# Optimization experiments

Measured on AMD Instinct MI355X. Metric: run time of the kernel, lower is better.

The kernel has to match this reference:

```python
import jax, jax.numpy as jnp
import numpy as np

H, E, DFF = 768, 8, 3072
B, S = 2, 1024


def setup_inputs() -> dict:
    key = jax.random.key(0)
    ks = jax.random.split(key, 4)
    scale = 1.0 / np.sqrt(H)
    return {
        "x": jax.random.normal(ks[0], (B, S, H), dtype=jnp.float32),
        "Wg": jax.random.normal(ks[1], (H, E), dtype=jnp.float32) * scale,
        "bg": jnp.zeros((E,), dtype=jnp.float32),
        "W1": jax.random.normal(ks[2], (E, H, DFF), dtype=jnp.float32) * scale,
        "b1": jnp.zeros((E, DFF), dtype=jnp.float32),
        "W2": jax.random.normal(ks[3], (E, DFF, H), dtype=jnp.float32) * (1.0 / np.sqrt(DFF)),
        "b2": jnp.zeros((E, H), dtype=jnp.float32),
        "top_k": 2,
    }


def reference(x, Wg, bg, W1, b1, W2, b2, top_k):
    b, s, h = x.shape
    xf = x.reshape(-1, h)                       # [T, H]
    logits = xf @ Wg + bg                        # [T, E]
    probs = jax.nn.softmax(logits, axis=-1)
    w, idx = jax.lax.top_k(probs, top_k)         # [T, K]
    w = w / jnp.sum(w, axis=-1, keepdims=True)   # renormalize top-k weights
    # dense combine weights per (token, expert): [T, E]
    comb = jnp.sum(jax.nn.one_hot(idx, W1.shape[0], dtype=xf.dtype) * w[..., None], axis=1)
    # per-expert MLP: Linear -> exact GELU -> Linear
    hmid = jax.nn.gelu(jnp.einsum('th,ehf->etf', xf, W1) + b1[:, None, :], approximate=False)
    eo = jnp.einsum('etf,efh->eth', hmid, W2) + b2[:, None, :]   # [E, T, H]
    out = jnp.einsum('te,eth->th', comb, eo)     # weighted combine
    return out.reshape(b, s, h)
```

## Files before the change

### kernel.cpp

```cpp
#include <hip/hip_runtime.h>
#include <hip/hip_bf16.h>
#include <math.h>

#define H_DIM 768
#define E_NUM 8
#define DFF   3072
#define T_NUM 2048
#define PAIRS 4096

typedef __attribute__((ext_vector_type(8))) short          s16x8;
typedef __attribute__((ext_vector_type(4))) float          f32x4;
typedef __attribute__((ext_vector_type(4))) unsigned int   u32x4;
typedef __attribute__((ext_vector_type(4))) unsigned short u16x4;
typedef __attribute__((ext_vector_type(8))) unsigned short u16x8;

__device__ __forceinline__ unsigned short f2bf(float f) {
  unsigned int u = __builtin_bit_cast(unsigned int, f);
  u += 0x7FFFu + ((u >> 16) & 1u);
  return (unsigned short)(u >> 16);
}

__device__ __forceinline__ float bf2f(unsigned short v) {
  unsigned int u = ((unsigned int)v) << 16;
  return __builtin_bit_cast(float, u);
}

__device__ __forceinline__ float gelu_fast(float x) {
  float t = x * x;
  float a = __builtin_fmaf(t, -0.10294221f, -2.3022082f);
  float w;
  asm("v_exp_f32 %0, %1" : "=v"(w) : "v"(x * a));
  float r;
  float d = 1.0f + w;
  asm("v_rcp_f32 %0, %1" : "=v"(r) : "v"(d));
  return x * r;
}


__device__ __forceinline__ void route_body(
    int rb, const float* __restrict__ x, const float* __restrict__ Wg,
    const float* __restrict__ bg, int* __restrict__ eidx, float* __restrict__ ew) {
  int wave = threadIdx.x >> 6, lane = threadIdx.x & 63;
  int t = rb * 4 + wave;
  const float* xr = x + (size_t)t * H_DIM;
  float acc[E_NUM];
#pragma unroll
  for (int e = 0; e < E_NUM; ++e) acc[e] = 0.f;
#pragma unroll
  for (int i = 0; i < H_DIM / 64; ++i) {
    int h = i * 64 + lane;
    float xv = xr[h];
    f32x4 w0 = *(const f32x4*)&Wg[h * 8];
    f32x4 w1 = *(const f32x4*)&Wg[h * 8 + 4];
    acc[0] += xv * w0[0]; acc[1] += xv * w0[1];
    acc[2] += xv * w0[2]; acc[3] += xv * w0[3];
    acc[4] += xv * w1[0]; acc[5] += xv * w1[1];
    acc[6] += xv * w1[2]; acc[7] += xv * w1[3];
  }
#pragma unroll
  for (int e = 0; e < E_NUM; ++e) {
#pragma unroll
    for (int off = 32; off > 0; off >>= 1) acc[e] += __shfl_xor(acc[e], off);
  }
  if (lane == 0) {
    float l[E_NUM];
#pragma unroll
    for (int e = 0; e < E_NUM; ++e) l[e] = acc[e] + bg[e];
    int i0 = 0;
#pragma unroll
    for (int e = 1; e < E_NUM; ++e) if (l[e] > l[i0]) i0 = e;
    int i1 = (i0 == 0) ? 1 : 0;
#pragma unroll
    for (int e = 0; e < E_NUM; ++e) if (e != i0 && l[e] > l[i1]) i1 = e;
    float d  = expf(l[i1] - l[i0]);
    eidx[2 * t]     = i0;
    eidx[2 * t + 1] = i1;
    ew[2 * t]       = 1.f / (1.f + d);
    ew[2 * t + 1]   = d / (1.f + d);
  }
}

__device__ __forceinline__ void transpose_body(
    int tb, const float* __restrict__ in, unsigned short* __restrict__ out,
    int R, int C) {
  __shared__ unsigned short tile[64][72];
  int e   = tb / ((R / 64) * (C / 64));
  int rem = tb % ((R / 64) * (C / 64));
  int bx  = rem % (C / 64);
  int by  = rem / (C / 64);
  int c0 = bx * 64, r0 = by * 64;
  const float* ip = in + (size_t)e * R * C;
  unsigned short* op = out + (size_t)e * R * C;
  int tid = threadIdx.x;
  int tx = tid & 15, ty = tid >> 4;
#pragma unroll
  for (int i = 0; i < 4; ++i) {
    int r = ty + 16 * i;
    f32x4 v = *(const f32x4*)&ip[(size_t)(r0 + r) * C + c0 + tx * 4];
    u16x4 o;
    o[0] = f2bf(v[0]); o[1] = f2bf(v[1]); o[2] = f2bf(v[2]); o[3] = f2bf(v[3]);
    *(u16x4*)&tile[r][tx * 4] = o;
  }
  __syncthreads();
  int c  = tid & 63;
  int rc = (tid >> 6) * 16;
#pragma unroll
  for (int h = 0; h < 2; ++h) {
    u16x8 o;
#pragma unroll
    for (int j = 0; j < 8; ++j) o[j] = tile[rc + h * 8 + j][c];
    *(u16x8*)&op[(size_t)(c0 + c) * R + r0 + rc + h * 8] = o;
  }
}

__device__ __forceinline__ void gather_body(
    int gb, const float* __restrict__ x, const int* __restrict__ tok_of,
    unsigned short* __restrict__ Xg) {
  int s = gb * 4 + (threadIdx.x >> 6);
  int lane = threadIdx.x & 63;
  int t = tok_of[s];
  const f32x4* xr = (const f32x4*)(x + (size_t)t * H_DIM);
  u16x4* orow = (u16x4*)(Xg + (size_t)s * H_DIM);
#pragma unroll
  for (int i = 0; i < H_DIM / 256; ++i) {
    f32x4 v = xr[i * 64 + lane];
    u16x4 o;
    o[0] = f2bf(v[0]); o[1] = f2bf(v[1]); o[2] = f2bf(v[2]); o[3] = f2bf(v[3]);
    orow[i * 64 + lane] = o;
  }
}


__global__ __launch_bounds__(256) void k_route_t1(
    const float* __restrict__ x, const float* __restrict__ Wg,
    const float* __restrict__ bg, int* __restrict__ eidx, float* __restrict__ ew,
    const float* __restrict__ W1, unsigned short* __restrict__ Wb1) {
  int b = blockIdx.x;
  if (b < T_NUM / 4) route_body(b, x, Wg, bg, eidx, ew);
  else               transpose_body(b - T_NUM / 4, W1, Wb1, H_DIM, DFF);
}

__global__ __launch_bounds__(256) void k_gather_t2(
    const float* __restrict__ x, const int* __restrict__ tok_of,
    unsigned short* __restrict__ Xg,
    const float* __restrict__ W2, unsigned short* __restrict__ Wb2) {
  int b = blockIdx.x;
  if (b < PAIRS / 4) gather_body(b, x, tok_of, Xg);
  else               transpose_body(b - PAIRS / 4, W2, Wb2, DFF, H_DIM);
}

__global__ __launch_bounds__(256) void k_build(
    const int* __restrict__ eidx, int* __restrict__ counts, int* __restrict__ offsets,
    int* __restrict__ tok_of, int* __restrict__ slot_of) {
  __shared__ int cnt[E_NUM];
  __shared__ int cur[E_NUM];
  int tid = threadIdx.x;
  if (tid < E_NUM) cnt[tid] = 0;
  __syncthreads();
#pragma unroll
  for (int i = 0; i < PAIRS / 256; ++i)
    atomicAdd(&cnt[eidx[i * 256 + tid]], 1);
  __syncthreads();
  if (tid == 0) {
    int s = 0;
    for (int e = 0; e < E_NUM; ++e) { cur[e] = s; s += cnt[e]; }
  }
  __syncthreads();
  if (tid < E_NUM) { counts[tid] = cnt[tid]; offsets[tid] = cur[tid]; }
#pragma unroll
  for (int i = 0; i < PAIRS / 256; ++i) {
    int p = i * 256 + tid;
    int s = atomicAdd(&cur[eidx[p]], 1);
    tok_of[s] = p >> 1;
    slot_of[p] = s;
  }
}

template <int KTOT, int NT, int NSPLIT, int MT_MAX, bool GELU_OUT>
__global__ __launch_bounds__(256) void k_gemm(
    const unsigned short* __restrict__ A, const unsigned short* __restrict__ B,
    const float* __restrict__ bias, void* __restrict__ C,
    const int* __restrict__ counts, const int* __restrict__ offsets) {
  constexpr int NDIM  = NT * 128;
  constexpr int KLEN  = KTOT / NSPLIT;
  constexpr int NSTEP = KLEN / 64;
  int l = blockIdx.x;
  int nt = l % NT;  l /= NT;
  int e  = l & 7;   l >>= 3;
  int part = l % NSPLIT;
  int mt = l / NSPLIT;
  int Me = counts[e];
  if (mt * 128 >= Me) return;
  int seg = offsets[e];

  __shared__ __align__(16) unsigned short Al[2][128 * 64];
  __shared__ __align__(16) unsigned short Bl[2][128 * 64];

  int tid  = threadIdx.x;
  int lane = tid & 63;
  int wave = tid >> 6;
  int wm = wave >> 1, wn = wave & 1;

  int sr   = tid >> 3;
  int scl  = (tid & 7) * 8;
  int scs  = (((tid & 7) ^ (sr & 7)) * 8);
  int rxor = (lane & 7) << 3;

  f32x4 acc[4][4];
#pragma unroll
  for (int m = 0; m < 4; ++m)
#pragma unroll
    for (int n = 0; n < 4; ++n) acc[m][n] = (f32x4){0.f, 0.f, 0.f, 0.f};

  const unsigned short* Abase = A + (size_t)seg * KTOT;
  const unsigned short* Bbase = B + (size_t)e * NDIM * KTOT + (size_t)(nt * 128) * KTOT;
  const int kbeg = part * KLEN;

  auto stage = [&](int bb, int k0) {
#pragma unroll
    for (int j = 0; j < 4; ++j) {
      int row = j * 32 + sr;
      int r = mt * 128 + row;
      r = (r < Me) ? r : (Me - 1);
      const unsigned short* gp = Abase + (size_t)r * KTOT + k0 + scs;
      __builtin_amdgcn_global_load_lds(
          (__attribute__((address_space(1))) void*)gp,
          (__attribute__((address_space(3))) void*)&Al[bb][row * 64 + scl], 16, 0, 0);
    }
#pragma unroll
    for (int j = 0; j < 4; ++j) {
      int row = j * 32 + sr;
      const unsigned short* gp = Bbase + (size_t)row * KTOT + k0 + scs;
      __builtin_amdgcn_global_load_lds(
          (__attribute__((address_space(1))) void*)gp,
          (__attribute__((address_space(3))) void*)&Bl[bb][row * 64 + scl], 16, 0, 0);
    }
  };

  auto compute = [&](int bb) {
#pragma unroll
    for (int kk = 0; kk < 2; ++kk) {
      int ko = kk * 32 + (lane >> 4) * 8;
      s16x8 af[4], bfr[4];
#pragma unroll
      for (int m = 0; m < 4; ++m) {
        int row = wm * 64 + m * 16 + (lane & 15);
        u32x4 v = *(const u32x4*)&Al[bb][(row * 64 + ko) ^ rxor];
        af[m] = __builtin_bit_cast(s16x8, v);
      }
#pragma unroll
      for (int n = 0; n < 4; ++n) {
        int row = wn * 64 + n * 16 + (lane & 15);
        u32x4 v = *(const u32x4*)&Bl[bb][(row * 64 + ko) ^ rxor];
        bfr[n] = __builtin_bit_cast(s16x8, v);
      }
#pragma unroll
      for (int m = 0; m < 4; ++m)
#pragma unroll
        for (int n = 0; n < 4; ++n)
          acc[m][n] = __builtin_amdgcn_mfma_f32_16x16x32_bf16(af[m], bfr[n], acc[m][n], 0, 0, 0);
    }
  };

  stage(0, kbeg);
  stage(1, kbeg + 64);
  int cur = 0;
#pragma unroll
  for (int s = 0; s < NSTEP; ++s) {
    if (s + 1 < NSTEP) asm volatile("s_waitcnt vmcnt(8)" ::: "memory");
    else               asm volatile("s_waitcnt vmcnt(0)" ::: "memory");
    __builtin_amdgcn_s_barrier();
    compute(cur);
    if (s + 2 < NSTEP) {
      __builtin_amdgcn_s_barrier();
      stage(cur, kbeg + (s + 2) * 64);
    }
    cur ^= 1;
  }

  int rbase = mt * 128 + wm * 64;
  int cbase = nt * 128 + wn * 64;
#pragma unroll
  for (int m = 0; m < 4; ++m) {
#pragma unroll
    for (int n = 0; n < 4; ++n) {
      int col = cbase + n * 16 + (lane & 15);
      float bv = GELU_OUT ? bias[e * NDIM + col] : 0.f;
#pragma unroll
      for (int r = 0; r < 4; ++r) {
        int row = rbase + m * 16 + (lane >> 4) * 4 + r;
        if (row < Me) {
          float v = acc[m][n][r] + bv;
          size_t idx = ((size_t)part * PAIRS + seg + row) * NDIM + col;
          if constexpr (GELU_OUT) {
            ((unsigned short*)C)[idx] = f2bf(gelu_fast(v));
          } else {
            ((unsigned short*)C)[idx] = f2bf(v);
          }
        }
      }
    }
  }
}

template <int NSPLIT>
__global__ void k_combine(const unsigned short* __restrict__ P, const int* __restrict__ slot_of,
                          const int* __restrict__ eidx, const float* __restrict__ ew,
                          const float* __restrict__ b2, float* __restrict__ out) {
  int t = blockIdx.x;
  int i = threadIdx.x;
  int s0 = slot_of[2 * t], s1 = slot_of[2 * t + 1];
  int e0 = eidx[2 * t],    e1 = eidx[2 * t + 1];
  float w0 = ew[2 * t], w1 = ew[2 * t + 1];
  f32x4 a = *(const f32x4*)&b2[e0 * H_DIM + i * 4];
  f32x4 c = *(const f32x4*)&b2[e1 * H_DIM + i * 4];
#pragma unroll
  for (int p = 0; p < NSPLIT; ++p) {
    u16x4 va = *(const u16x4*)&P[((size_t)p * PAIRS + s0) * H_DIM + i * 4];
    u16x4 vb = *(const u16x4*)&P[((size_t)p * PAIRS + s1) * H_DIM + i * 4];
#pragma unroll
    for (int j = 0; j < 4; ++j) { a[j] += bf2f(va[j]); c[j] += bf2f(vb[j]); }
  }
  f32x4 o;
  o[0] = w0 * a[0] + w1 * c[0];
  o[1] = w0 * a[1] + w1 * c[1];
  o[2] = w0 * a[2] + w1 * c[2];
  o[3] = w0 * a[3] + w1 * c[3];
  ((f32x4*)(out + (size_t)t * H_DIM))[i] = o;
}

extern "C" void kernel_launch(void* const* d_in, const int* in_sizes, int n_in,
                              void* d_out, int out_size, void* d_ws, size_t ws_size,
                              hipStream_t stream) {
  (void)in_sizes; (void)n_in; (void)out_size;
  const float* x  = (const float*)d_in[0];
  const float* Wg = (const float*)d_in[1];
  const float* bg = (const float*)d_in[2];
  const float* W1 = (const float*)d_in[3];
  const float* b1 = (const float*)d_in[4];
  const float* W2 = (const float*)d_in[5];
  const float* b2 = (const float*)d_in[6];
  float* out = (float*)d_out;

  char* w = (char*)d_ws;
  size_t off = 0;
  auto take = [&](size_t n) { void* p = w + off; off = (off + n + 255) & ~(size_t)255; return p; };
  int*   ctrl    = (int*)  take(64 * sizeof(int));
  int*   eidx    = (int*)  take(PAIRS * sizeof(int));
  float* ew      = (float*)take(PAIRS * sizeof(float));
  int*   slot_of = (int*)  take(PAIRS * sizeof(int));
  int*   tok_of  = (int*)  take(PAIRS * sizeof(int));
  unsigned short* Xg   = (unsigned short*)take((size_t)PAIRS * H_DIM * 2);
  unsigned short* Hmid = (unsigned short*)take((size_t)PAIRS * DFF * 2);
  unsigned short* P    = (unsigned short*)take((size_t)3 * PAIRS * H_DIM * 2);
  unsigned short* Wb1  = (unsigned short*)take((size_t)E_NUM * H_DIM * DFF * 2);
  unsigned short* Wb2  = (unsigned short*)take((size_t)E_NUM * H_DIM * DFF * 2);
  if (off > ws_size) return;

  int* counts  = ctrl;
  int* offsets = ctrl + 8;

  k_route_t1<<<T_NUM / 4 + E_NUM * (H_DIM / 64) * (DFF / 64), 256, 0, stream>>>(
      x, Wg, bg, eidx, ew, W1, Wb1);
  k_build<<<1, 256, 0, stream>>>(eidx, counts, offsets, tok_of, slot_of);
  k_gather_t2<<<PAIRS / 4 + E_NUM * (DFF / 64) * (H_DIM / 64), 256, 0, stream>>>(
      x, tok_of, Xg, W2, Wb2);

  k_gemm<H_DIM, DFF / 128, 1, 8, true><<<(DFF / 128) * E_NUM * 8, 256, 0, stream>>>(
      Xg, Wb1, b1, Hmid, counts, offsets);

  k_gemm<DFF, H_DIM / 128, 3, 8, false><<<(H_DIM / 128) * E_NUM * 3 * 8, 256, 0, stream>>>(
      Hmid, Wb2, b2, P, counts, offsets);
  k_combine<3><<<T_NUM, 192, 0, stream>>>(P, slot_of, eidx, ew, b2, out);
}
```

Baseline: 152.0 us.

## Use 256x256 eight-wave GEMM tiles with interleaved LDS reads, staging and MFMA

Replaces the 128x128, 4-wave grouped GEMM with a 256x256, 512-thread kernel in which each wave owns a 128x64 sub-tile. The k-loop is split into four MFMA quadrants, with LDS fragment reads and global-to-LDS staging of the next k-slab placed between them. Each quadrant is separated by barriers and wrapped in s_setprio so loads overlap with matrix math. The second GEMM's split-K goes from 3 to 4, and the combine step and the partial-sum buffer are resized to match. Larger tiles raise operand reuse and cut B-weight traffic, but the grid now only covers 3 M-tiles (768 rows) per expert, so more heavily loaded experts would silently drop rows, and fewer blocks may leave CUs idle.

```diff
diff --git a/kernel.cpp b/kernel.cpp
--- a/kernel.cpp
+++ b/kernel.cpp
@@ -177,111 +177,149 @@
 }
 
 template <int KTOT, int NT, int NSPLIT, int MT_MAX, bool GELU_OUT>
-__global__ __launch_bounds__(256) void k_gemm(
+__global__ __launch_bounds__(512) void k_gemm8(
     const unsigned short* __restrict__ A, const unsigned short* __restrict__ B,
     const float* __restrict__ bias, void* __restrict__ C,
     const int* __restrict__ counts, const int* __restrict__ offsets) {
-  constexpr int NDIM  = NT * 128;
+  constexpr int NDIM  = NT * 256;
   constexpr int KLEN  = KTOT / NSPLIT;
   constexpr int NSTEP = KLEN / 64;
+  static_assert(NSTEP >= 3, "pipeline depth");
   int l = blockIdx.x;
   int nt = l % NT;  l /= NT;
   int e  = l & 7;   l >>= 3;
   int part = l % NSPLIT;
   int mt = l / NSPLIT;
   int Me = counts[e];
-  if (mt * 128 >= Me) return;
+  if (mt * 256 >= Me) return;
   int seg = offsets[e];
 
-  __shared__ __align__(16) unsigned short Al[2][128 * 64];
-  __shared__ __align__(16) unsigned short Bl[2][128 * 64];
+  __shared__ __align__(16) unsigned short Al[2][256 * 64];
+  __shared__ __align__(16) unsigned short Bl[2][256 * 64];
 
   int tid  = threadIdx.x;
   int lane = tid & 63;
   int wave = tid >> 6;
-  int wm = wave >> 1, wn = wave & 1;
-
-  int sr   = tid >> 3;
-  int scl  = (tid & 7) * 8;
-  int scs  = (((tid & 7) ^ (sr & 7)) * 8);
+  int wm = wave >> 2, wn = wave & 3;
+
+  int srow   = tid >> 3;
+  int schunk = tid & 7;
+  int scs  = ((schunk ^ (srow & 7)) * 8);
+  int scl  = schunk * 8;
   int rxor = (lane & 7) << 3;
 
-  f32x4 acc[4][4];
-#pragma unroll
-  for (int m = 0; m < 4; ++m)
+  f32x4 acc[8][4];
+#pragma unroll
+  for (int m = 0; m < 8; ++m)
 #pragma unroll
     for (int n = 0; n < 4; ++n) acc[m][n] = (f32x4){0.f, 0.f, 0.f, 0.f};
 
   const unsigned short* Abase = A + (size_t)seg * KTOT;
-  const unsigned short* Bbase = B + (size_t)e * NDIM * KTOT + (size_t)(nt * 128) * KTOT;
+  const unsigned short* Bbase = B + (size_t)e * NDIM * KTOT + (size_t)(nt * 256) * KTOT;
   const int kbeg = part * KLEN;
 
-  auto stage = [&](int bb, int k0) {
-#pragma unroll
-    for (int j = 0; j < 4; ++j) {
-      int row = j * 32 + sr;
-      int r = mt * 128 + row;
+  auto stageA = [&](int d, int k0) {
+#pragma unroll
+    for (int p = 0; p < 4; ++p) {
+      int row = p * 64 + srow;
+      int r = mt * 256 + row;
       r = (r < Me) ? r : (Me - 1);
       const unsigned short* gp = Abase + (size_t)r * KTOT + k0 + scs;
       __builtin_amdgcn_global_load_lds(
           (__attribute__((address_space(1))) void*)gp,
-          (__attribute__((address_space(3))) void*)&Al[bb][row * 64 + scl], 16, 0, 0);
+          (__attribute__((address_space(3))) void*)&Al[d][row * 64 + scl], 16, 0, 0);
     }
-#pragma unroll
-    for (int j = 0; j < 4; ++j) {
-      int row = j * 32 + sr;
+  };
+  auto stageB = [&](int d, int k0) {
+#pragma unroll
+    for (int p = 0; p < 4; ++p) {
+      int row = p * 64 + srow;
       const unsigned short* gp = Bbase + (size_t)row * KTOT + k0 + scs;
       __builtin_amdgcn_global_load_lds(
           (__attribute__((address_space(1))) void*)gp,
-          (__attribute__((address_space(3))) void*)&Bl[bb][row * 64 + scl], 16, 0, 0);
+          (__attribute__((address_space(3))) void*)&Bl[d][row * 64 + scl], 16, 0, 0);
     }
   };
 
-  auto compute = [&](int bb) {
-#pragma unroll
-    for (int kk = 0; kk < 2; ++kk) {
-      int ko = kk * 32 + (lane >> 4) * 8;
-      s16x8 af[4], bfr[4];
-#pragma unroll
-      for (int m = 0; m < 4; ++m) {
-        int row = wm * 64 + m * 16 + (lane & 15);
-        u32x4 v = *(const u32x4*)&Al[bb][(row * 64 + ko) ^ rxor];
-        af[m] = __builtin_bit_cast(s16x8, v);
+  s16x8 af[4][2], bf0[2][2], bf1[2][2];
+  auto readA = [&](int d, int mh) {
+#pragma unroll
+    for (int m = 0; m < 4; ++m)
+#pragma unroll
+      for (int kk = 0; kk < 2; ++kk) {
+        int row = wm * 128 + (mh * 4 + m) * 16 + (lane & 15);
+        int ko  = kk * 32 + (lane >> 4) * 8;
+        u32x4 v = *(const u32x4*)&Al[d][(row * 64 + ko) ^ rxor];
+        af[m][kk] = __builtin_bit_cast(s16x8, v);
       }
-#pragma unroll
-      for (int n = 0; n < 4; ++n) {
-        int row = wn * 64 + n * 16 + (lane & 15);
-        u32x4 v = *(const u32x4*)&Bl[bb][(row * 64 + ko) ^ rxor];
-        bfr[n] = __builtin_bit_cast(s16x8, v);
+  };
+  auto readB = [&](int d, int nh, s16x8 (&bf)[2][2]) {
+#pragma unroll
+    for (int n = 0; n < 2; ++n)
+#pragma unroll
+      for (int kk = 0; kk < 2; ++kk) {
+        int row = wn * 64 + (nh * 2 + n) * 16 + (lane & 15);
+        int ko  = kk * 32 + (lane >> 4) * 8;
+        u32x4 v = *(const u32x4*)&Bl[d][(row * 64 + ko) ^ rxor];
+        bf[n][kk] = __builtin_bit_cast(s16x8, v);
       }
-#pragma unroll
-      for (int m = 0; m < 4; ++m)
-#pragma unroll
-        for (int n = 0; n < 4; ++n)
-          acc[m][n] = __builtin_amdgcn_mfma_f32_16x16x32_bf16(af[m], bfr[n], acc[m][n], 0, 0, 0);
-    }
   };
-
-  stage(0, kbeg);
-  stage(1, kbeg + 64);
-  int cur = 0;
-#pragma unroll
-  for (int s = 0; s < NSTEP; ++s) {
-    if (s + 1 < NSTEP) asm volatile("s_waitcnt vmcnt(8)" ::: "memory");
-    else               asm volatile("s_waitcnt vmcnt(0)" ::: "memory");
-    __builtin_amdgcn_s_barrier();
-    compute(cur);
-    if (s + 2 < NSTEP) {
-      __builtin_amdgcn_s_barrier();
-      stage(cur, kbeg + (s + 2) * 64);
-    }
-    cur ^= 1;
-  }
-
-  int rbase = mt * 128 + wm * 64;
-  int cbase = nt * 128 + wn * 64;
-#pragma unroll
-  for (int m = 0; m < 4; ++m) {
+  auto mfmaq = [&](int mh, int nh, s16x8 (&bf)[2][2]) {
+#pragma unroll
+    for (int m = 0; m < 4; ++m)
+#pragma unroll
+      for (int n = 0; n < 2; ++n)
+#pragma unroll
+        for (int kk = 0; kk < 2; ++kk)
+          acc[mh * 4 + m][nh * 2 + n] = __builtin_amdgcn_mfma_f32_16x16x32_bf16(
+              af[m][kk], bf[n][kk], acc[mh * 4 + m][nh * 2 + n], 0, 0, 0);
+  };
+
+  stageB(0, kbeg);       stageA(0, kbeg);
+  stageB(1, kbeg + 64);  stageA(1, kbeg + 64);
+  asm volatile("s_waitcnt vmcnt(8)" ::: "memory");
+  __builtin_amdgcn_s_barrier();
+
+#pragma unroll 2
+  for (int t = 0; t < NSTEP; ++t) {
+    int d = t & 1;
+    int kn = kbeg + (t + 2) * 64;
+    readA(d, 0); readB(d, 0, bf0);
+    __builtin_amdgcn_s_barrier();
+    asm volatile("s_waitcnt lgkmcnt(0)" ::: "memory");
+    __builtin_amdgcn_s_setprio(1);
+    mfmaq(0, 0, bf0);
+    __builtin_amdgcn_s_setprio(0);
+    __builtin_amdgcn_s_barrier();
+    readB(d, 1, bf1);
+    __builtin_amdgcn_s_barrier();
+    asm volatile("s_waitcnt lgkmcnt(0)" ::: "memory");
+    __builtin_amdgcn_s_setprio(1);
+    mfmaq(0, 1, bf1);
+    __builtin_amdgcn_s_setprio(0);
+    __builtin_amdgcn_s_barrier();
+    readA(d, 1);
+    if (t + 2 < NSTEP) stageB(d, kn);
+    __builtin_amdgcn_s_barrier();
+    asm volatile("s_waitcnt lgkmcnt(0)" ::: "memory");
+    __builtin_amdgcn_s_setprio(1);
+    mfmaq(1, 1, bf1);
+    __builtin_amdgcn_s_setprio(0);
+    __builtin_amdgcn_s_barrier();
+    if (t + 2 < NSTEP) stageA(d, kn);
+    __builtin_amdgcn_s_barrier();
+    __builtin_amdgcn_s_setprio(1);
+    mfmaq(1, 0, bf0);
+    __builtin_amdgcn_s_setprio(0);
+    if (t + 2 < NSTEP)      asm volatile("s_waitcnt vmcnt(8)" ::: "memory");
+    else if (t + 1 < NSTEP) asm volatile("s_waitcnt vmcnt(0)" ::: "memory");
+    __builtin_amdgcn_s_barrier();
+  }
+
+  int rbase = mt * 256 + wm * 128;
+  int cbase = nt * 256 + wn * 64;
+#pragma unroll
+  for (int m = 0; m < 8; ++m) {
 #pragma unroll
     for (int n = 0; n < 4; ++n) {
       int col = cbase + n * 16 + (lane & 15);
@@ -352,7 +390,7 @@
   int*   tok_of  = (int*)  take(PAIRS * sizeof(int));
   unsigned short* Xg   = (unsigned short*)take((size_t)PAIRS * H_DIM * 2);
   unsigned short* Hmid = (unsigned short*)take((size_t)PAIRS * DFF * 2);
-  unsigned short* P    = (unsigned short*)take((size_t)3 * PAIRS * H_DIM * 2);
+  unsigned short* P    = (unsigned short*)take((size_t)4 * PAIRS * H_DIM * 2);
   unsigned short* Wb1  = (unsigned short*)take((size_t)E_NUM * H_DIM * DFF * 2);
   unsigned short* Wb2  = (unsigned short*)take((size_t)E_NUM * H_DIM * DFF * 2);
   if (off > ws_size) return;
@@ -366,10 +404,10 @@
   k_gather_t2<<<PAIRS / 4 + E_NUM * (DFF / 64) * (H_DIM / 64), 256, 0, stream>>>(
       x, tok_of, Xg, W2, Wb2);
 
-  k_gemm<H_DIM, DFF / 128, 1, 8, true><<<(DFF / 128) * E_NUM * 8, 256, 0, stream>>>(
+  k_gemm8<H_DIM, DFF / 256, 1, 3, true><<<(DFF / 256) * E_NUM * 3, 512, 0, stream>>>(
       Xg, Wb1, b1, Hmid, counts, offsets);
 
-  k_gemm<DFF, H_DIM / 128, 3, 8, false><<<(H_DIM / 128) * E_NUM * 3 * 8, 256, 0, stream>>>(
+  k_gemm8<DFF, H_DIM / 256, 4, 3, false><<<(H_DIM / 256) * E_NUM * 4 * 3, 512, 0, stream>>>(
       Hmid, Wb2, b2, P, counts, offsets);
-  k_combine<3><<<T_NUM, 192, 0, stream>>>(P, slot_of, eidx, ew, b2, out);
-}
+  k_combine<4><<<T_NUM, 192, 0, stream>>>(P, slot_of, eidx, ew, b2, out);
+}
```

After: 169.6 us. 1.12x slower.
